# Performance work log

Measured on AMD Instinct MI355X. Metric: run time of the kernel, lower is better.

Reference implementation:

```python
import jax, jax.numpy as jnp
import numpy as np

B, L, D, H, HD = 2, 8192, 1024, 16, 64
MINI = 64
NC = L // MINI
TTT_BASE_LR = 1.0
NUM_CHUNKS = 4
TEXT_LEN = 64
INIT_OFFSET = 2048


def setup_inputs() -> dict:
    key = jax.random.key(0)
    ks = jax.random.split(key, 16)
    hidden_states = jax.random.normal(ks[0], (B, L, D), dtype=jnp.float32)
    # llama-style rope table as (cos, sin) pairs: [L, HD//2, 2]
    inv_freq = 1.0 / (10000.0 ** (np.arange(0, HD, 2, dtype=np.float32) / HD))
    t = np.arange(L, dtype=np.float32)
    ang = np.outer(t, inv_freq)  # [L, HD//2]
    freqs_cis = jnp.asarray(np.stack([np.cos(ang), np.sin(ang)], axis=-1))
    std = 0.02
    inp = {"hidden_states": hidden_states, "freqs_cis": freqs_cis}
    names = ["wq", "wk", "wv", "wu"]
    for i, n in enumerate(names):
        inp[n + "_w"] = jax.random.normal(ks[1 + i], (D, D), dtype=jnp.float32) * std  # [in, out]
        inp[n + "_b"] = jnp.zeros((D,), dtype=jnp.float32)
    inp["ttt_norm_weight"] = jnp.ones((H, HD), dtype=jnp.float32)
    inp["ttt_norm_bias"] = jnp.zeros((H, HD), dtype=jnp.float32)
    inp["lr_weight"] = jax.random.normal(ks[6], (H, 1, D), dtype=jnp.float32) * std
    inp["lr_bias"] = jnp.zeros((H, 1), dtype=jnp.float32)
    return inp


def _l2norm(x):
    return x / jnp.maximum(jnp.linalg.norm(x, axis=-1, keepdims=True), 1e-12)


def _rope(x, cos, sin):
    # x: [B, L, H, HD]; cos/sin: [L, HD//2] -> broadcast [1, L, 1, HD//2]
    c = cos[None, :, None, :]
    s = sin[None, :, None, :]
    xr, xi = x[..., 0::2], x[..., 1::2]
    out_r = xr * c - xi * s
    out_i = xr * s + xi * c
    return jnp.stack([out_r, out_i], axis=-1).reshape(x.shape)


def _interleave(x):
    # x: [B, H, NC, C, F]; splice text chunks into video scenes (static offsets)
    b, h, nc, c, f = x.shape
    xf = x.reshape(b, h, nc * c, f)
    stl = TEXT_LEN * NUM_CHUNKS
    x_text = xf[:, :, :stl]
    x_video = xf[:, :, stl:]
    texts = jnp.split(x_text, NUM_CHUNKS, axis=2)
    vio = INIT_OFFSET - TEXT_LEN
    vids = [x_video[:, :, :vio]] + list(jnp.split(x_video[:, :, vio:], NUM_CHUNKS - 1, axis=2))
    pieces = [jnp.concatenate([texts[i], vids[i]], axis=2) for i in range(NUM_CHUNKS)]
    return jnp.concatenate(pieces, axis=2).reshape(b, h, nc, c, f)


def reference(hidden_states, freqs_cis, wq_w, wq_b, wk_w, wk_b, wv_w, wv_b,
              wu_w, wu_b, ttt_norm_weight, ttt_norm_bias, lr_weight, lr_bias):
    X = hidden_states  # [B, L, D]
    XQ = (X @ wq_w + wq_b).reshape(B, L, H, HD)
    XK = (X @ wk_w + wk_b).reshape(B, L, H, HD)
    XV = (X @ wv_w + wv_b).reshape(B, L, H, HD)
    XU = (X @ wu_w + wu_b).reshape(B, L, H, HD)

    XQ, XK, XU = _l2norm(XQ), _l2norm(XK), _l2norm(XU)

    # seq_text_length = 0 in process_input -> rope over the whole sequence
    cos, sin = freqs_cis[..., 0], freqs_cis[..., 1]
    XQ = _rope(XQ, cos, sin)
    XK = _rope(XK, cos, sin)
    XU = _rope(XU, cos, sin)

    # ln reconstruction target (std uses Bessel correction like torch.std)
    diff = XV - XK
    mean = diff.mean(axis=-1, keepdims=True)
    std = jnp.std(diff, axis=-1, keepdims=True, ddof=1)
    norm = (diff - mean) / (std + 1e-8)
    XV = ttt_norm_weight[None, None] * norm + ttt_norm_bias[None, None] + XK

    # reshape to mini-batches: [B, H, NC, C, HD]
    def to_mb(t):
        return t.transpose(0, 2, 1, 3).reshape(B, H, NC, MINI, HD)
    XQ, XK, XV, XU = to_mb(XQ), to_mb(XK), to_mb(XV), to_mb(XU)
    Xmb = X.reshape(B, NC, MINI, D)

    # per-head LR gating
    ttt_lr = jnp.einsum('bnkc,hdc->bhnkd', Xmb, lr_weight) + lr_bias.reshape(1, -1, 1, 1, 1)
    ttt_lr = jax.nn.sigmoid(ttt_lr).transpose(0, 1, 2, 4, 3)  # [B, H, NC, 1, C]
    ttt_lr = TTT_BASE_LR * ttt_lr / HD
    eta = (1.0 / MINI) * jnp.tile(ttt_lr, (1, 1, 1, MINI, 1))  # [B, H, NC, C, C]

    XQ, XK, XV, XU = _interleave(XQ), _interleave(XK), _interleave(XV), _interleave(XU)
    eta = _interleave(eta)

    # HD == MINI == 64 so all five stack cleanly
    return jnp.stack([XQ, XK, XV, XU, eta], axis=0)
```

## Files before the change

### kernel.cpp

```cpp
#include <hip/hip_runtime.h>

typedef unsigned int u32;
typedef unsigned short u16;
typedef short short8v __attribute__((ext_vector_type(8)));
typedef float f32x4 __attribute__((ext_vector_type(4)));

#define ND 1024
#define NH 16
#define OUT_T ((size_t)16777216)

__device__ __forceinline__ u16 f2bf(float f) {
  u32 u = __float_as_uint(f);
  u32 r = u + 0x7fffu + ((u >> 16) & 1u);
  return (u16)(r >> 16);
}

__device__ __forceinline__ short8v pack8(float4 a, float4 b) {
  short8v v;
  v[0] = (short)f2bf(a.x); v[1] = (short)f2bf(a.y);
  v[2] = (short)f2bf(a.z); v[3] = (short)f2bf(a.w);
  v[4] = (short)f2bf(b.x); v[5] = (short)f2bf(b.y);
  v[6] = (short)f2bf(b.z); v[7] = (short)f2bf(b.w);
  return v;
}

__device__ __forceinline__ void gload16(const void* g, void* l) {
  __builtin_amdgcn_global_load_lds((const __attribute__((address_space(1))) void*)g,
                                   (__attribute__((address_space(3))) void*)l, 16, 0, 0);
}

__global__ void k_wt(const float* __restrict__ w0, const float* __restrict__ w1,
                     const float* __restrict__ w2, const float* __restrict__ w3,
                     u16* __restrict__ WT) {
  __shared__ float T[64][65];
  int bid = blockIdx.x;
  int w = bid >> 8;
  int tk = (bid >> 4) & 15, tc = bid & 15;
  const float* W = w == 0 ? w0 : w == 1 ? w1 : w == 2 ? w2 : w3;
  int k0 = tk << 6, c0 = tc << 6;
  int tid = threadIdx.x;
  for (int it = 0; it < 16; ++it) {
    int idx = it * 256 + tid;
    int kk = idx >> 6, cc = idx & 63;
    T[kk][cc] = W[(size_t)(k0 + kk) * ND + c0 + cc];
  }
  __syncthreads();
  for (int it = 0; it < 2; ++it) {
    int ci = it * 256 + tid;
    int cc = ci >> 3, k8 = ci & 7;
    int c = c0 + cc;
    short8v v;
    for (int j = 0; j < 8; ++j) v[j] = (short)f2bf(T[k8 * 8 + j][cc]);
    int stored = (k8 & 4) | ((k8 ^ (c >> 1)) & 3);
    size_t off = ((size_t)(w * ND + c) << 10) + k0 + (stored << 3);
    *(short8v*)(WT + off) = v;
  }
}

__global__ void k_xbf(const float* __restrict__ X, u16* __restrict__ Xb) {
  size_t i = ((size_t)blockIdx.x * 256 + threadIdx.x) * 8;
  float4 a = *(const float4*)(X + i), b = *(const float4*)(X + i + 4);
  *(short8v*)(Xb + i) = pack8(a, b);
}

__global__ __launch_bounds__(256) void k_lr2(const u16* __restrict__ Xb,
                                             const float* __restrict__ LW,
                                             const float* __restrict__ LB,
                                             float* __restrict__ out) {
  __shared__ __align__(16) char smem[46080];
  u16* LWs = (u16*)smem;
  u16* As = (u16*)(smem + 32768);
  float* El = (float*)(smem + 40960);
  const int tid = threadIdx.x, lane = tid & 63, wid = tid >> 6;
  const int l15 = lane & 15, lg = lane >> 4;
  const int n = blockIdx.x;
  const int tok0 = n << 6;

  {
    int row = tid >> 4;
    int cbase = (tid & 15) << 3;
    const float* src = LW + row * ND + (cbase << 3);
    for (int i = 0; i < 8; ++i) {
      float4 a = *(const float4*)(src + i * 8);
      float4 b = *(const float4*)(src + i * 8 + 4);
      int sc = (cbase + i) ^ (row & 7);
      *(short8v*)(LWs + row * 1024 + (sc << 3)) = pack8(a, b);
    }
  }

  const int arow0 = (wid << 4) + (lane >> 3);
  const u16* asrc = Xb + (size_t)(tok0 + arow0) * ND + ((((lane & 7) ^ arow0) & 7) << 3);
  const u32 aldo = wid << 10;
  const int aoff = ((wid << 4) + l15) << 6;
  const int key = l15 & 7;

  f32x4 acc;
  for (int r = 0; r < 4; ++r) acc[r] = 0.f;
  __syncthreads();

  for (int kt = 0; kt < 16; ++kt) {
    gload16(asrc + (kt << 6), As + aldo);
    gload16(asrc + (kt << 6) + 8 * ND, As + aldo + 512);
    __syncthreads();
    for (int ks = 0; ks < 2; ++ks) {
      int kcl = (ks << 2) + lg;
      int kcg = (kt << 3) + kcl;
      short8v af = *(const short8v*)(As + aoff + ((kcl ^ key) << 3));
      short8v bf = *(const short8v*)(LWs + (l15 << 10) + ((kcg ^ key) << 3));
      acc = __builtin_amdgcn_mfma_f32_16x16x32_bf16(af, bf, acc, 0, 0, 0);
    }
    __syncthreads();
  }

  for (int rr = 0; rr < 4; ++rr) {
    float v = acc[rr] + LB[l15];
    float e = (1.f / (1.f + expf(-v))) * (1.f / 4096.f);
    El[l15 * 72 + (wid << 4) + (lg << 2) + rr] = e;
  }
  __syncthreads();

  const int b = n >> 7, nl = n & 127;
  int q, rc;
  if (nl < 4) { q = nl; rc = 0; }
  else { q = (nl - 4) / 31; rc = nl - 3 - 31 * q; }
  const int pc = q * 32 + rc;
  const int j = tid >> 2, kq = tid & 3;
  size_t base = 4 * OUT_T + (((size_t)(b * NH) << 13) + (pc << 6)) * 64 + (size_t)j * 64;
  for (int h = 0; h < 16; ++h) {
    float* po = out + base + ((size_t)h << 19);
    for (int qq = 0; qq < 4; ++qq) {
      int k0 = (kq + (qq << 2)) << 2;
      const float* ep = El + h * 72 + k0;
      f32x4 t; t[0] = ep[0]; t[1] = ep[1]; t[2] = ep[2]; t[3] = ep[3];
      *(f32x4*)(po + k0) = t;
    }
  }
}

__global__ __launch_bounds__(512, 4) void k_main(
    const u16* __restrict__ Xb, const float* __restrict__ FC,
    const u16* __restrict__ WT,
    const float* __restrict__ qb, const float* __restrict__ kb,
    const float* __restrict__ vb, const float* __restrict__ ub,
    const float* __restrict__ tw, const float* __restrict__ tb,
    float* __restrict__ out) {
  __shared__ __align__(16) char smem[49152];
  float* Cs = (float*)smem;

  const int tid = threadIdx.x;
  const int lane = tid & 63;
  const int wid = tid >> 6;
  const int wm = wid >> 2, wn = wid & 3;
  const int l15 = lane & 15, lg = lane >> 4;
  const int xcd = blockIdx.x & 7;
  const int local = blockIdx.x >> 3;
  const int h = (xcd << 1) | (local >> 7);
  const int s0 = (local & 127) << 7;

  f32x4 acc[4][4];
  for (int i = 0; i < 4; ++i)
    for (int j = 0; j < 4; ++j)
      for (int r = 0; r < 4; ++r) acc[i][j][r] = 0.f;

  const float* bp = (wn == 0) ? qb : (wn == 1) ? kb : (wn == 2) ? vb : ub;
  float biasv[4];
  for (int fn = 0; fn < 4; ++fn) biasv[fn] = bp[h * 64 + fn * 16 + l15];

  const int rS = tid >> 2;
  const int chp = tid & 3;
  const u16* asrc = Xb + (size_t)(s0 + rS) * ND + ((chp ^ ((rS >> 1) & 3)) << 3);
  const u16* bsrc = WT + (((size_t)((rS >> 6) * ND + h * 64 + (rS & 63))) << 10) + (chp << 3);
  const u32 aldo = wid << 9;
  const u32 bldo = wid << 9;

  int aoff[4], akey[4], boff[4], bkey[4];
  for (int f = 0; f < 4; ++f) {
    int ra = (wm << 6) + (f << 4) + l15;
    aoff[f] = ra << 5; akey[f] = (ra >> 1) & 3;
    int rb = (wn << 6) + (f << 4) + l15;
    boff[f] = rb << 5; bkey[f] = (rb >> 1) & 3;
  }

  {
    u16* ad = (u16*)smem;
    u16* bd = (u16*)(smem + 8192);
    gload16(asrc, ad + aldo);
    gload16(bsrc, bd + bldo);
    gload16(bsrc + 2097152, bd + bldo + 4096);
  }
  __syncthreads();

  for (int kt = 0; kt < 32; ++kt) {
    const int cur = kt & 1;
    if (kt < 31) {
      const int k0n = (kt + 1) << 5;
      u16* ad = (u16*)(smem + ((cur ^ 1) ? 24576 : 0));
      u16* bd = ad + 4096;
      gload16(asrc + k0n, ad + aldo);
      gload16(bsrc + k0n, bd + bldo);
      gload16(bsrc + k0n + 2097152, bd + bldo + 4096);
    }
    const u16* As = (const u16*)(smem + (cur ? 24576 : 0));
    const u16* Bs = As + 4096;
    short8v af[4], bf[4];
#pragma unroll
    for (int f = 0; f < 4; ++f)
      af[f] = *(const short8v*)(As + aoff[f] + ((lg ^ akey[f]) << 3));
#pragma unroll
    for (int f = 0; f < 4; ++f)
      bf[f] = *(const short8v*)(Bs + boff[f] + ((lg ^ bkey[f]) << 3));
    __builtin_amdgcn_s_setprio(1);
#pragma unroll
    for (int fm = 0; fm < 4; ++fm)
#pragma unroll
      for (int fn = 0; fn < 4; ++fn)
        acc[fm][fn] = __builtin_amdgcn_mfma_f32_16x16x32_bf16(
            af[fm], bf[fn], acc[fm][fn], 0, 0, 0);
    __builtin_amdgcn_s_setprio(0);
    __syncthreads();
  }

  for (int ph = 0; ph < 4; ++ph) {
    if (wm == (ph >> 1)) {
      for (int f2 = 0; f2 < 2; ++f2) {
        int fm = ((ph & 1) << 1) + f2;
        for (int fn = 0; fn < 4; ++fn)
          for (int rr = 0; rr < 4; ++rr) {
            int rl = (f2 << 4) + (lg << 2) + rr;
            int col = (wn << 6) + (fn << 4) + l15;
            Cs[rl * 261 + col] = acc[fm][fn][rr] + biasv[fn];
          }
      }
    }
    __syncthreads();
    {
      int tloc = tid >> 4, o = tid & 15;
      int dbase = o << 2;
      int stok = s0 + (ph << 5) + tloc;
      int b = stok >> 13, seq = stok & 8191;
      const float* crow = Cs + tloc * 261;
      f32x4 fc = *(const f32x4*)(FC + ((size_t)seq << 6) + dbase);
      f32x4 vq = *(const f32x4*)(crow + dbase);
      f32x4 vk = *(const f32x4*)(crow + 64 + dbase);
      f32x4 vv = *(const f32x4*)(crow + 128 + dbase);
      f32x4 vu = *(const f32x4*)(crow + 192 + dbase);
      float sq = 0.f, sk = 0.f, su = 0.f;
      for (int j = 0; j < 4; ++j) {
        sq += vq[j] * vq[j]; sk += vk[j] * vk[j]; su += vu[j] * vu[j];
      }
      sq += __shfl_xor(sq, 1); sq += __shfl_xor(sq, 2);
      sq += __shfl_xor(sq, 4); sq += __shfl_xor(sq, 8);
      sk += __shfl_xor(sk, 1); sk += __shfl_xor(sk, 2);
      sk += __shfl_xor(sk, 4); sk += __shfl_xor(sk, 8);
      su += __shfl_xor(su, 1); su += __shfl_xor(su, 2);
      su += __shfl_xor(su, 4); su += __shfl_xor(su, 8);
      float qi = 1.f / fmaxf(sqrtf(sq), 1e-12f);
      float ki = 1.f / fmaxf(sqrtf(sk), 1e-12f);
      float ui = 1.f / fmaxf(sqrtf(su), 1e-12f);
      int p;
      if (seq < 256) p = ((seq >> 6) << 11) + (seq & 63);
      else { int v = seq - 256; int qc = v / 1984; p = (qc << 11) + 64 + (v - qc * 1984); }
      float* po = out + ((((size_t)(b * NH + h) << 13) + p) << 6) + dbase;
      f32x4 kr;
      kr[0] = vk[0] * ki * fc[0] - vk[1] * ki * fc[1];
      kr[1] = vk[0] * ki * fc[1] + vk[1] * ki * fc[0];
      kr[2] = vk[2] * ki * fc[2] - vk[3] * ki * fc[3];
      kr[3] = vk[2] * ki * fc[3] + vk[3] * ki * fc[2];
      *(f32x4*)(po + OUT_T) = kr;
      f32x4 df;
      float sd = 0.f, sdd = 0.f;
      for (int j = 0; j < 4; ++j) {
        df[j] = vv[j] - kr[j];
        sd += df[j]; sdd += df[j] * df[j];
      }
      sd += __shfl_xor(sd, 1); sd += __shfl_xor(sd, 2);
      sd += __shfl_xor(sd, 4); sd += __shfl_xor(sd, 8);
      sdd += __shfl_xor(sdd, 1); sdd += __shfl_xor(sdd, 2);
      sdd += __shfl_xor(sdd, 4); sdd += __shfl_xor(sdd, 8);
      float mean = sd * (1.f / 64.f);
      float var = (sdd - sd * sd * (1.f / 64.f)) * (1.f / 63.f);
      float istd = 1.f / (sqrtf(fmaxf(var, 0.f)) + 1e-8f);
      f32x4 twv = *(const f32x4*)(tw + h * 64 + dbase);
      f32x4 tbv = *(const f32x4*)(tb + h * 64 + dbase);
      f32x4 vo;
      for (int j = 0; j < 4; ++j)
        vo[j] = twv[j] * ((df[j] - mean) * istd) + tbv[j] + kr[j];
      *(f32x4*)(po + 2 * OUT_T) = vo;
      f32x4 qr;
      qr[0] = vq[0] * qi * fc[0] - vq[1] * qi * fc[1];
      qr[1] = vq[0] * qi * fc[1] + vq[1] * qi * fc[0];
      qr[2] = vq[2] * qi * fc[2] - vq[3] * qi * fc[3];
      qr[3] = vq[2] * qi * fc[3] + vq[3] * qi * fc[2];
      *(f32x4*)po = qr;
      qr[0] = vu[0] * ui * fc[0] - vu[1] * ui * fc[1];
      qr[1] = vu[0] * ui * fc[1] + vu[1] * ui * fc[0];
      qr[2] = vu[2] * ui * fc[2] - vu[3] * ui * fc[3];
      qr[3] = vu[2] * ui * fc[3] + vu[3] * ui * fc[2];
      *(f32x4*)(po + 3 * OUT_T) = qr;
    }
    __syncthreads();
  }
}

extern "C" void kernel_launch(void* const* d_in, const int* in_sizes, int n_in,
                              void* d_out, int out_size, void* d_ws, size_t ws_size,
                              hipStream_t stream) {
  const float* X  = (const float*)d_in[0];
  const float* FC = (const float*)d_in[1];
  const float* wq = (const float*)d_in[2];
  const float* qb = (const float*)d_in[3];
  const float* wk = (const float*)d_in[4];
  const float* kb = (const float*)d_in[5];
  const float* wv = (const float*)d_in[6];
  const float* vb = (const float*)d_in[7];
  const float* wu = (const float*)d_in[8];
  const float* ub = (const float*)d_in[9];
  const float* tw = (const float*)d_in[10];
  const float* tb = (const float*)d_in[11];
  const float* lw = (const float*)d_in[12];
  const float* lb = (const float*)d_in[13];
  float* out = (float*)d_out;
  u16* WT = (u16*)d_ws;
  u16* Xb = (u16*)((char*)d_ws + (8u << 20));

  hipLaunchKernelGGL(k_wt, dim3(1024), dim3(256), 0, stream, wq, wk, wv, wu, WT);
  hipLaunchKernelGGL(k_xbf, dim3(8192), dim3(256), 0, stream, X, Xb);
  hipLaunchKernelGGL(k_lr2, dim3(256), dim3(256), 0, stream, Xb, lw, lb, out);
  hipLaunchKernelGGL(k_main, dim3(2048), dim3(512), 0, stream,
                     Xb, FC, WT, qb, kb, vb, ub, tw, tb, out);
}
```

Baseline: 251.8 us.

## Load weight fragments directly to registers and shrink main GEMM block to four waves

The weight transpose kernel now writes B in an MFMA-fragment-ready layout, so the main kernel loads each wave's B operands straight from global memory into registers, double-buffered one k-step ahead, instead of staging them through LDS. The block drops from 8 to 4 waves. Each wave covers all 128 rows of one projection (q/k/v/u) with 8x4 accumulators, and the epilogue runs in 8 phases of 16 tokens. This removes LDS traffic and footprint for B, but raises register pressure and cuts waves per block, which may lower latency hiding.

Result: faster. 234.0 us (-7.1%).

```diff
diff --git a/kernel.cpp b/kernel.cpp
--- a/kernel.cpp
+++ b/kernel.cpp
@@ -48,11 +48,9 @@
   for (int it = 0; it < 2; ++it) {
     int ci = it * 256 + tid;
     int cc = ci >> 3, k8 = ci & 7;
-    int c = c0 + cc;
     short8v v;
     for (int j = 0; j < 8; ++j) v[j] = (short)f2bf(T[k8 * 8 + j][cc]);
-    int stored = (k8 & 4) | ((k8 ^ (c >> 1)) & 3);
-    size_t off = ((size_t)(w * ND + c) << 10) + k0 + (stored << 3);
+    size_t off = ((((size_t)(w * 16 + tc) * 128) + (tk << 3) + k8) * 64 + cc) * 8;
     *(short8v*)(WT + off) = v;
   }
 }
@@ -137,56 +135,56 @@
   }
 }
 
-__global__ __launch_bounds__(512, 4) void k_main(
+__global__ __launch_bounds__(256, 2) void k_main(
     const u16* __restrict__ Xb, const float* __restrict__ FC,
     const u16* __restrict__ WT,
     const float* __restrict__ qb, const float* __restrict__ kb,
     const float* __restrict__ vb, const float* __restrict__ ub,
     const float* __restrict__ tw, const float* __restrict__ tb,
     float* __restrict__ out) {
-  __shared__ __align__(16) char smem[49152];
+  __shared__ __align__(16) char smem[16896];
   float* Cs = (float*)smem;
 
   const int tid = threadIdx.x;
   const int lane = tid & 63;
-  const int wid = tid >> 6;
-  const int wm = wid >> 2, wn = wid & 3;
+  const int w = tid >> 6;
   const int l15 = lane & 15, lg = lane >> 4;
   const int xcd = blockIdx.x & 7;
   const int local = blockIdx.x >> 3;
   const int h = (xcd << 1) | (local >> 7);
   const int s0 = (local & 127) << 7;
 
-  f32x4 acc[4][4];
-  for (int i = 0; i < 4; ++i)
+  f32x4 acc[8][4];
+  for (int i = 0; i < 8; ++i)
     for (int j = 0; j < 4; ++j)
       for (int r = 0; r < 4; ++r) acc[i][j][r] = 0.f;
 
-  const float* bp = (wn == 0) ? qb : (wn == 1) ? kb : (wn == 2) ? vb : ub;
+  const float* bp = (w == 0) ? qb : (w == 1) ? kb : (w == 2) ? vb : ub;
   float biasv[4];
   for (int fn = 0; fn < 4; ++fn) biasv[fn] = bp[h * 64 + fn * 16 + l15];
 
-  const int rS = tid >> 2;
-  const int chp = tid & 3;
+  const int rS = (w << 5) + (lane >> 2);
+  const int chp = lane & 3;
   const u16* asrc = Xb + (size_t)(s0 + rS) * ND + ((chp ^ ((rS >> 1) & 3)) << 3);
-  const u16* bsrc = WT + (((size_t)((rS >> 6) * ND + h * 64 + (rS & 63))) << 10) + (chp << 3);
-  const u32 aldo = wid << 9;
-  const u32 bldo = wid << 9;
-
-  int aoff[4], akey[4], boff[4], bkey[4];
-  for (int f = 0; f < 4; ++f) {
-    int ra = (wm << 6) + (f << 4) + l15;
+  const u32 aldo = w << 10;
+
+  const u16* Bg = WT + (((size_t)(w * 16 + h)) << 16);
+
+  int aoff[8], akey[8];
+  for (int f = 0; f < 8; ++f) {
+    int ra = (f << 4) + l15;
     aoff[f] = ra << 5; akey[f] = (ra >> 1) & 3;
-    int rb = (wn << 6) + (f << 4) + l15;
-    boff[f] = rb << 5; bkey[f] = (rb >> 1) & 3;
-  }
-
+  }
+
+  gload16(asrc, (u16*)smem + aldo);
+  gload16(asrc + 16 * ND, (u16*)smem + aldo + 512);
+  short8v bc0, bc1, bc2, bc3, bn0, bn1, bn2, bn3;
   {
-    u16* ad = (u16*)smem;
-    u16* bd = (u16*)(smem + 8192);
-    gload16(asrc, ad + aldo);
-    gload16(bsrc, bd + bldo);
-    gload16(bsrc + 2097152, bd + bldo + 4096);
+    const u16* bb = Bg + ((lg * 64 + l15) << 3);
+    bc0 = *(const short8v*)(bb);
+    bc1 = *(const short8v*)(bb + 128);
+    bc2 = *(const short8v*)(bb + 256);
+    bc3 = *(const short8v*)(bb + 384);
   }
   __syncthreads();
 
@@ -194,49 +192,46 @@
     const int cur = kt & 1;
     if (kt < 31) {
       const int k0n = (kt + 1) << 5;
-      u16* ad = (u16*)(smem + ((cur ^ 1) ? 24576 : 0));
-      u16* bd = ad + 4096;
+      u16* ad = (u16*)smem + ((cur ^ 1) << 12);
       gload16(asrc + k0n, ad + aldo);
-      gload16(bsrc + k0n, bd + bldo);
-      gload16(bsrc + k0n + 2097152, bd + bldo + 4096);
-    }
-    const u16* As = (const u16*)(smem + (cur ? 24576 : 0));
-    const u16* Bs = As + 4096;
-    short8v af[4], bf[4];
+      gload16(asrc + k0n + 16 * ND, ad + aldo + 512);
+      const u16* bb = Bg + ((((kt + 1) << 2) + lg) << 9) + (l15 << 3);
+      bn0 = *(const short8v*)(bb);
+      bn1 = *(const short8v*)(bb + 128);
+      bn2 = *(const short8v*)(bb + 256);
+      bn3 = *(const short8v*)(bb + 384);
+    }
+    const u16* As = (const u16*)smem + (cur << 12);
+    short8v af[8];
 #pragma unroll
-    for (int f = 0; f < 4; ++f)
+    for (int f = 0; f < 8; ++f)
       af[f] = *(const short8v*)(As + aoff[f] + ((lg ^ akey[f]) << 3));
-#pragma unroll
-    for (int f = 0; f < 4; ++f)
-      bf[f] = *(const short8v*)(Bs + boff[f] + ((lg ^ bkey[f]) << 3));
     __builtin_amdgcn_s_setprio(1);
 #pragma unroll
-    for (int fm = 0; fm < 4; ++fm)
+    for (int fm = 0; fm < 8; ++fm) {
+      acc[fm][0] = __builtin_amdgcn_mfma_f32_16x16x32_bf16(af[fm], bc0, acc[fm][0], 0, 0, 0);
+      acc[fm][1] = __builtin_amdgcn_mfma_f32_16x16x32_bf16(af[fm], bc1, acc[fm][1], 0, 0, 0);
+      acc[fm][2] = __builtin_amdgcn_mfma_f32_16x16x32_bf16(af[fm], bc2, acc[fm][2], 0, 0, 0);
+      acc[fm][3] = __builtin_amdgcn_mfma_f32_16x16x32_bf16(af[fm], bc3, acc[fm][3], 0, 0, 0);
+    }
+    __builtin_amdgcn_s_setprio(0);
+    __syncthreads();
+    bc0 = bn0; bc1 = bn1; bc2 = bn2; bc3 = bn3;
+  }
+
 #pragma unroll
-      for (int fn = 0; fn < 4; ++fn)
-        acc[fm][fn] = __builtin_amdgcn_mfma_f32_16x16x32_bf16(
-            af[fm], bf[fn], acc[fm][fn], 0, 0, 0);
-    __builtin_amdgcn_s_setprio(0);
-    __syncthreads();
-  }
-
-  for (int ph = 0; ph < 4; ++ph) {
-    if (wm == (ph >> 1)) {
-      for (int f2 = 0; f2 < 2; ++f2) {
-        int fm = ((ph & 1) << 1) + f2;
-        for (int fn = 0; fn < 4; ++fn)
-          for (int rr = 0; rr < 4; ++rr) {
-            int rl = (f2 << 4) + (lg << 2) + rr;
-            int col = (wn << 6) + (fn << 4) + l15;
-            Cs[rl * 261 + col] = acc[fm][fn][rr] + biasv[fn];
-          }
+  for (int ph = 0; ph < 8; ++ph) {
+    for (int fn = 0; fn < 4; ++fn)
+      for (int rr = 0; rr < 4; ++rr) {
+        int rl = (lg << 2) + rr;
+        int col = (w << 6) + (fn << 4) + l15;
+        Cs[rl * 261 + col] = acc[ph][fn][rr] + biasv[fn];
       }
-    }
     __syncthreads();
     {
       int tloc = tid >> 4, o = tid & 15;
       int dbase = o << 2;
-      int stok = s0 + (ph << 5) + tloc;
+      int stok = s0 + (ph << 4) + tloc;
       int b = stok >> 13, seq = stok & 8191;
       const float* crow = Cs + tloc * 261;
       f32x4 fc = *(const f32x4*)(FC + ((size_t)seq << 6) + dbase);
@@ -326,6 +321,6 @@
   hipLaunchKernelGGL(k_wt, dim3(1024), dim3(256), 0, stream, wq, wk, wv, wu, WT);
   hipLaunchKernelGGL(k_xbf, dim3(8192), dim3(256), 0, stream, X, Xb);
   hipLaunchKernelGGL(k_lr2, dim3(256), dim3(256), 0, stream, Xb, lw, lb, out);
-  hipLaunchKernelGGL(k_main, dim3(2048), dim3(512), 0, stream,
+  hipLaunchKernelGGL(k_main, dim3(2048), dim3(256), 0, stream,
                      Xb, FC, WT, qb, kb, vb, ub, tw, tb, out);
 }
```
